# Kernel tuning notes

Measured on AMD Instinct MI355X. Metric: run time of the kernel, lower is better.

The kernel has to match this reference:

```python
import jax, jax.numpy as jnp
import numpy as np

N_NODES = 100000
N_EDGES = 1600000
IN_SIZE = 512
HID_SIZE = 256
OUT_SIZE = 16
DROP_P = 0.5


def _degrees(idx, n):
    d = jax.ops.segment_sum(jnp.ones(idx.shape[0], jnp.float32), idx, num_segments=n)
    return jnp.maximum(d, 1.0)  # DGL clamps zero degrees to 1


def graph_conv(src, dst, feat, W, b, activation=None):
    # DGL GraphConv, norm='both': D_in^{-1/2} A D_out^{-1/2} X W + b
    n = feat.shape[0]
    inv_sqrt_dout = _degrees(src, n) ** -0.5   # out-degree of source nodes
    inv_sqrt_din = _degrees(dst, n) ** -0.5    # in-degree of destination nodes
    h = feat * inv_sqrt_dout[:, None]
    h = h @ W  # in_feats >= out_feats -> transform before aggregation (same math)
    # message passing: scatter-add source messages to destinations
    h = jax.ops.segment_sum(h[src], dst, num_segments=n)
    h = h * inv_sqrt_din[:, None] + b
    if activation is not None:
        h = activation(h)
    return h


def setup_inputs() -> dict:
    key = jax.random.key(0)
    ks = jax.random.split(key, 9)
    features = jax.random.normal(ks[0], (N_NODES, IN_SIZE), jnp.float32)
    src = jax.random.randint(ks[1], (N_EDGES,), 0, N_NODES)
    dst = jax.random.randint(ks[2], (N_EDGES,), 0, N_NODES)
    W1 = jax.random.normal(ks[3], (IN_SIZE, HID_SIZE), jnp.float32) / np.sqrt(IN_SIZE).astype(np.float32)
    b1 = jnp.zeros((HID_SIZE,), jnp.float32)
    W2 = jax.random.normal(ks[4], (HID_SIZE, HID_SIZE), jnp.float32) / np.sqrt(HID_SIZE).astype(np.float32)
    b2 = jnp.zeros((HID_SIZE,), jnp.float32)
    W3 = jax.random.normal(ks[5], (HID_SIZE, OUT_SIZE), jnp.float32) / np.sqrt(HID_SIZE).astype(np.float32)
    b3 = jnp.zeros((OUT_SIZE,), jnp.float32)
    return {"features": features, "src": src, "dst": dst,
            "W1": W1, "b1": b1, "W2": W2, "b2": b2, "W3": W3, "b3": b3}


def reference(features, src, dst, W1, b1, W2, b2, W3, b3):
    # layer 0: GraphConv + relu
    h = graph_conv(src, dst, features, W1, b1, activation=jax.nn.relu)
    # dropout(0.5) before layer 1 (deterministic fixed-key mask, training semantics)
    keep = jax.random.bernoulli(jax.random.key(42), 1.0 - DROP_P, h.shape)
    h = jnp.where(keep, h / (1.0 - DROP_P), 0.0)
    # layer 1: GraphConv (no activation)
    h = graph_conv(src, dst, h, W2, b2, activation=None)
    # layer 2: plain Linear head
    return h @ W3 + b3
```

## Files before the change

kernel.cpp:

```cpp
#include <hip/hip_runtime.h>
#include <stdint.h>

#define NN    100000
#define NE    1600000
#define IN_F  512
#define HID   256
#define OUTF  16
#define NPAD  100096
#define NBK   391
#define EPB   8192

typedef unsigned int u32;
typedef __bf16 bfrag  __attribute__((ext_vector_type(8)));
typedef float  f32x4  __attribute__((ext_vector_type(4)));
typedef short  s16x8  __attribute__((ext_vector_type(8)));

__device__ __forceinline__ u32 rotl32(u32 x, int r){ return (x<<r)|(x>>(32-r)); }

__device__ __forceinline__ bool drop_keep(u32 i){
    const u32 ks0 = 0u, ks1 = 42u, ks2 = 0x1BD11BDAu ^ 0u ^ 42u;
    u32 x0 = 0u + ks0;
    u32 x1 = i  + ks1;
#define TFR(r) { x0 += x1; x1 = rotl32(x1,(r)); x1 ^= x0; }
    TFR(13) TFR(15) TFR(26) TFR(6)   x0 += ks1; x1 += ks2 + 1u;
    TFR(17) TFR(29) TFR(16) TFR(24)  x0 += ks2; x1 += ks0 + 2u;
    TFR(13) TFR(15) TFR(26) TFR(6)   x0 += ks0; x1 += ks1 + 3u;
    TFR(17) TFR(29) TFR(16) TFR(24)  x0 += ks1; x1 += ks2 + 4u;
    TFR(13) TFR(15) TFR(26) TFR(6)   x0 += ks2; x1 += ks0 + 5u;
#undef TFR
    return ((x0 ^ x1) >> 31) == 0u;
}

__device__ __forceinline__ short f2b(float f){
    union { float f; u32 u; } v; v.f = f;
    u32 r = (v.u + 0x7FFFu + ((v.u >> 16) & 1u)) >> 16;
    return (short)r;
}
__device__ __forceinline__ float blo(u32 u){ union{u32 u; float f;} v; v.u = u << 16;         return v.f; }
__device__ __forceinline__ float bhi(u32 u){ union{u32 u; float f;} v; v.u = u & 0xFFFF0000u; return v.f; }

__device__ __forceinline__ u32 cvt_pk_bf16(float lo, float hi){
    u32 r;
    asm("v_cvt_pk_bf16_f32 %0, %1, %2" : "=v"(r) : "v"(lo), "v"(hi));
    return r;
}

__device__ __forceinline__ void gll16(const void* g, void* l){
    __builtin_amdgcn_global_load_lds((const __attribute__((address_space(1))) void*)g,
                                     (__attribute__((address_space(3))) void*)l, 16, 0, 0);
}


__global__ __launch_bounds__(256) void build_hist(const int4* __restrict__ src4,
                                                  const int4* __restrict__ dst4,
                                                  int* deg_out, int* __restrict__ bcnt){
    __shared__ int h[NBK];
    int t = threadIdx.x;
    for (int i = t; i < NBK; i += 256) h[i] = 0;
    __syncthreads();
    for (int i = blockIdx.x * 256 + t; i < NE / 4; i += gridDim.x * 256) {
        int4 s = src4[i];
        int4 d = dst4[i];
        atomicAdd(&deg_out[s.x], 1);
        atomicAdd(&deg_out[s.y], 1);
        atomicAdd(&deg_out[s.z], 1);
        atomicAdd(&deg_out[s.w], 1);
        atomicAdd(&h[d.x >> 8], 1);
        atomicAdd(&h[d.y >> 8], 1);
        atomicAdd(&h[d.z >> 8], 1);
        atomicAdd(&h[d.w >> 8], 1);
    }
    __syncthreads();
    for (int i = t; i < NBK; i += 256)
        if (h[i]) atomicAdd(&bcnt[i], h[i]);
}

__global__ __launch_bounds__(256) void finalize_deg(const int* __restrict__ deg_out,
                                                    const int* __restrict__ row_ptr,
                                                    float* isdo, float* isdi){
    int i = blockIdx.x * blockDim.x + threadIdx.x;
    if (i < NN) {
        isdo[i] = rsqrtf(fmaxf((float)deg_out[i], 1.0f));
        isdi[i] = rsqrtf(fmaxf((float)(row_ptr[i + 1] - row_ptr[i]), 1.0f));
    }
}

__global__ __launch_bounds__(512) void bucket_scan(const int* __restrict__ bcnt,
                                                   int* __restrict__ bbase,
                                                   int* __restrict__ bcur,
                                                   int* __restrict__ row_ptr){
    __shared__ int sh[512];
    int t = threadIdx.x;
    int v = (t < NBK) ? bcnt[t] : 0;
    sh[t] = v;
    __syncthreads();
    for (int off = 1; off < 512; off <<= 1) {
        int a = (t >= off) ? sh[t - off] : 0;
        __syncthreads();
        sh[t] += a;
        __syncthreads();
    }
    int excl = sh[t] - v;
    if (t < NBK) { bbase[t] = excl; bcur[t] = excl; }
    if (t == 0)  { bbase[NBK] = NE; row_ptr[NN] = NE; }
}

__global__ __launch_bounds__(256) void bucket_scatter(const int* __restrict__ src,
                                                      const int* __restrict__ dst,
                                                      int* bcur, u32* __restrict__ tmp){
    __shared__ int lh[NBK];
    __shared__ int lb[NBK];
    int t = threadIdx.x;
    for (int i = t; i < NBK; i += 256) lh[i] = 0;
    __syncthreads();
    const int e0 = blockIdx.x * EPB;
    for (int k = t * 4; k < EPB; k += 1024) {
        int e = e0 + k;
        if (e < NE) {
            int4 d = *(const int4*)(dst + e);
            atomicAdd(&lh[d.x >> 8], 1);
            atomicAdd(&lh[d.y >> 8], 1);
            atomicAdd(&lh[d.z >> 8], 1);
            atomicAdd(&lh[d.w >> 8], 1);
        }
    }
    __syncthreads();
    for (int i = t; i < NBK; i += 256) {
        int c = lh[i];
        if (c) lb[i] = atomicAdd(&bcur[i], c);
        lh[i] = 0;
    }
    __syncthreads();
    for (int k = t * 4; k < EPB; k += 1024) {
        int e = e0 + k;
        if (e < NE) {
            int4 d = *(const int4*)(dst + e);
            int4 s = *(const int4*)(src + e);
            int b0 = d.x >> 8, b1 = d.y >> 8, b2 = d.z >> 8, b3 = d.w >> 8;
            int r0 = atomicAdd(&lh[b0], 1);
            tmp[lb[b0] + r0] = ((u32)s.x << 8) | ((u32)d.x & 255u);
            int r1 = atomicAdd(&lh[b1], 1);
            tmp[lb[b1] + r1] = ((u32)s.y << 8) | ((u32)d.y & 255u);
            int r2 = atomicAdd(&lh[b2], 1);
            tmp[lb[b2] + r2] = ((u32)s.z << 8) | ((u32)d.z & 255u);
            int r3 = atomicAdd(&lh[b3], 1);
            tmp[lb[b3] + r3] = ((u32)s.w << 8) | ((u32)d.w & 255u);
        }
    }
}

__global__ __launch_bounds__(256) void bucket_finalize(const u32* __restrict__ tmp,
                                                       const int* __restrict__ bbase,
                                                       int* __restrict__ row_ptr,
                                                       int* __restrict__ col_src){
    __shared__ int h[256];
    __shared__ int wtot[4];
    const int t = threadIdx.x;
    const int b = blockIdx.x;
    const int base = bbase[b];
    const int cnt  = bbase[b + 1] - base;
    h[t] = 0;
    __syncthreads();
    for (int k = t; k < cnt; k += 256)
        atomicAdd(&h[tmp[base + k] & 255u], 1);
    __syncthreads();
    int v = h[t];
    int lane = t & 63, w = t >> 6;
    int s = v;
    #pragma unroll
    for (int off = 1; off < 64; off <<= 1) {
        int u = __shfl_up(s, off);
        if (lane >= off) s += u;
    }
    if (lane == 63) wtot[w] = s;
    __syncthreads();
    int woff = 0;
    #pragma unroll
    for (int i = 0; i < 4; ++i) woff += (i < w) ? wtot[i] : 0;
    int excl = woff + s - v;
    int d = (b << 8) + t;
    if (d < NN) row_ptr[d] = base + excl;
    h[t] = excl;
    __syncthreads();
    for (int k = t; k < cnt; k += 256) {
        u32 p = tmp[base + k];
        int r = atomicAdd(&h[p & 255u], 1);
        col_src[base + r] = (int)(p >> 8);
    }
}


template<int Kd, int Nd>
__global__ __launch_bounds__(256) void convert_wt(const float* __restrict__ W,
                                                  short* __restrict__ WT){
    int i = blockIdx.x * 256 + threadIdx.x;
    if (i >= Kd * Nd) return;
    int n = i / Kd, k = i - n * Kd;
    WT[i] = f2b(W[(size_t)k * Nd + n]);
}

__global__ __launch_bounds__(256) void gemm_x(const float* __restrict__ X,
                                              const short* __restrict__ BT,
                                              const float* __restrict__ isdo,
                                              short* __restrict__ C){
    __shared__ __align__(16) float As[2 * 4160];
    __shared__ __align__(16) short Bs[2 * 8320];

    const int t = threadIdx.x;
    const int wave = t >> 6, lane = t & 63;
    const int bm = blockIdx.x * 128;

    const float* paA[4];
    #pragma unroll
    for (int g = 0; g < 4; ++g) {
        int row = bm + wave * 32 + g * 8 + (lane >> 3);
        if (row > NN - 1) row = NN - 1;
        paA[g] = X + (size_t)row * IN_F + (lane & 7) * 4;
    }
    const short* paB[4];
    #pragma unroll
    for (int g = 0; g < 4; ++g) {
        int col = (wave * 4 + g) * 16 + (lane >> 2);
        paB[g] = BT + (size_t)col * IN_F + (lane & 3) * 8;
    }

    const int wr = (wave >> 1) * 64;
    const int wc = (wave & 1) * 128;
    const int kq = lane >> 4, r15 = lane & 15;

    f32x4 acc[4][8];
    #pragma unroll
    for (int m = 0; m < 4; ++m)
        #pragma unroll
        for (int n = 0; n < 8; ++n) acc[m][n] = (f32x4)0.0f;

#define STAGE_X(BUF, K0) { \
    float* dA = As + (BUF) * 4160 + wave * 1040; \
    gll16(paA[0] + (K0), dA);       gll16(paA[1] + (K0), dA + 260); \
    gll16(paA[2] + (K0), dA + 520); gll16(paA[3] + (K0), dA + 780); \
    short* dB = Bs + (BUF) * 8320 + wave * 2080; \
    gll16(paB[0] + (K0), dB);        gll16(paB[1] + (K0), dB + 520); \
    gll16(paB[2] + (K0), dB + 1040); gll16(paB[3] + (K0), dB + 1560); }

#define COMPUTE_X(BUF) { \
    const float* AsC = As + (BUF) * 4160; \
    const short* BsC = Bs + (BUF) * 8320; \
    bfrag af[4], bfg[8]; \
    _Pragma("unroll") \
    for (int m = 0; m < 4; ++m) { \
        int r  = wr + m * 16 + r15; \
        const float* ap = AsC + (r >> 3) * 260 + (r & 7) * 32 + kq * 8; \
        float4 f0 = *(const float4*)ap; \
        float4 f1 = *(const float4*)(ap + 4); \
        uint4 q = make_uint4(cvt_pk_bf16(f0.x, f0.y), cvt_pk_bf16(f0.z, f0.w), \
                             cvt_pk_bf16(f1.x, f1.y), cvt_pk_bf16(f1.z, f1.w)); \
        af[m] = *(bfrag*)&q; \
    } \
    _Pragma("unroll") \
    for (int n = 0; n < 8; ++n) { \
        int cg = (wc >> 4) + n; \
        bfg[n] = *(const bfrag*)(BsC + cg * 520 + r15 * 32 + kq * 8); \
    } \
    _Pragma("unroll") \
    for (int m = 0; m < 4; ++m) \
        _Pragma("unroll") \
        for (int n = 0; n < 8; ++n) \
            acc[m][n] = __builtin_amdgcn_mfma_f32_16x16x32_bf16(af[m], bfg[n], acc[m][n], 0, 0, 0); }

    const int NT = IN_F / 32;
    STAGE_X(0, 0);
    int cur = 0;
    for (int tt = 0; tt < NT - 1; ++tt) {
        STAGE_X(cur ^ 1, (tt + 1) * 32);
        asm volatile("s_waitcnt vmcnt(8)" ::: "memory");
        __builtin_amdgcn_s_barrier();
        COMPUTE_X(cur);
        asm volatile("" ::: "memory");
        __builtin_amdgcn_s_barrier();
        cur ^= 1;
    }
    asm volatile("s_waitcnt vmcnt(0)" ::: "memory");
    __builtin_amdgcn_s_barrier();
    COMPUTE_X(cur);
#undef STAGE_X
#undef COMPUTE_X

    const int crow0 = bm + wr + (lane >> 4) * 4;
    const int ccol0 = wc + r15;
    #pragma unroll
    for (int m = 0; m < 4; ++m)
        #pragma unroll
        for (int r = 0; r < 4; ++r) {
            int row = crow0 + m * 16 + r;
            float sc = (row < NN) ? isdo[row] : 0.0f;
            #pragma unroll
            for (int n = 0; n < 8; ++n)
                C[(size_t)row * HID + ccol0 + n * 16] = f2b(acc[m][n][r] * sc);
        }
}

template<int K>
__global__ __launch_bounds__(256) void gemm_bt(const short* __restrict__ A,
                                               const short* __restrict__ BT,
                                               short* __restrict__ C){
    __shared__ __align__(16) short As[2 * 4160];
    __shared__ __align__(16) short Bs[2 * 8320];

    const int t = threadIdx.x;
    const int wave = t >> 6, lane = t & 63;
    const int bm = blockIdx.x * 128;

    const short* paA[2];
    #pragma unroll
    for (int g = 0; g < 2; ++g) {
        int row = bm + (wave * 2 + g) * 16 + (lane >> 2);
        paA[g] = A + (size_t)row * K + (lane & 3) * 8;
    }
    const short* paB[4];
    #pragma unroll
    for (int g = 0; g < 4; ++g) {
        int col = (wave * 4 + g) * 16 + (lane >> 2);
        paB[g] = BT + (size_t)col * K + (lane & 3) * 8;
    }

    const int wr = (wave >> 1) * 64;
    const int wc = (wave & 1) * 128;
    const int kq = lane >> 4, r15 = lane & 15;

    f32x4 acc[4][8];
    #pragma unroll
    for (int m = 0; m < 4; ++m)
        #pragma unroll
        for (int n = 0; n < 8; ++n) acc[m][n] = (f32x4)0.0f;

#define STAGE_B(BUF, K0) { \
    short* dA = As + (BUF) * 4160 + wave * 1040; \
    gll16(paA[0] + (K0), dA); gll16(paA[1] + (K0), dA + 520); \
    short* dB = Bs + (BUF) * 8320 + wave * 2080; \
    gll16(paB[0] + (K0), dB);        gll16(paB[1] + (K0), dB + 520); \
    gll16(paB[2] + (K0), dB + 1040); gll16(paB[3] + (K0), dB + 1560); }

#define COMPUTE_B(BUF) { \
    const short* AsC = As + (BUF) * 4160; \
    const short* BsC = Bs + (BUF) * 8320; \
    bfrag af[4], bfg[8]; \
    _Pragma("unroll") \
    for (int m = 0; m < 4; ++m) { \
        int ch = (wr + m * 16) >> 4; \
        af[m] = *(const bfrag*)(AsC + ch * 520 + r15 * 32 + kq * 8); \
    } \
    _Pragma("unroll") \
    for (int n = 0; n < 8; ++n) { \
        int cg = (wc >> 4) + n; \
        bfg[n] = *(const bfrag*)(BsC + cg * 520 + r15 * 32 + kq * 8); \
    } \
    _Pragma("unroll") \
    for (int m = 0; m < 4; ++m) \
        _Pragma("unroll") \
        for (int n = 0; n < 8; ++n) \
            acc[m][n] = __builtin_amdgcn_mfma_f32_16x16x32_bf16(af[m], bfg[n], acc[m][n], 0, 0, 0); }

    const int NT = K / 32;
    STAGE_B(0, 0);
    int cur = 0;
    for (int tt = 0; tt < NT - 1; ++tt) {
        STAGE_B(cur ^ 1, (tt + 1) * 32);
        asm volatile("s_waitcnt vmcnt(6)" ::: "memory");
        __builtin_amdgcn_s_barrier();
        COMPUTE_B(cur);
        asm volatile("" ::: "memory");
        __builtin_amdgcn_s_barrier();
        cur ^= 1;
    }
    asm volatile("s_waitcnt vmcnt(0)" ::: "memory");
    __builtin_amdgcn_s_barrier();
    COMPUTE_B(cur);
#undef STAGE_B
#undef COMPUTE_B

    const int crow0 = bm + wr + (lane >> 4) * 4;
    const int ccol0 = wc + r15;
    #pragma unroll
    for (int m = 0; m < 4; ++m)
        #pragma unroll
        for (int n = 0; n < 8; ++n)
            #pragma unroll
            for (int r = 0; r < 4; ++r)
                C[(size_t)(crow0 + m * 16 + r) * HID + ccol0 + n * 16] = f2b(acc[m][n][r]);
}

template<int MODE>
__global__ __launch_bounds__(256) void gather_agg(const short* __restrict__ H,
                                                  const int* __restrict__ rp,
                                                  const int* __restrict__ cs,
                                                  const float* __restrict__ isdi,
                                                  const float* __restrict__ isdo,
                                                  const float* __restrict__ bias,
                                                  short* __restrict__ out){
    const int lane = threadIdx.x & 63;
    const int node = __builtin_amdgcn_readfirstlane((int)(blockIdx.x * 4) + (int)(threadIdx.x >> 6));
    const int e0  = rp[node];
    const int end = rp[node + 1];
    const int sub = lane & 31, half = lane >> 5;
    const u32 off16 = (u32)sub * 16u;
    const char* Hb = (const char*)H;

    float a[8] = {0,0,0,0,0,0,0,0};
    float b[8] = {0,0,0,0,0,0,0,0};

#define LD4(s) (*(const uint4*)(Hb + ((((u32)(s)) << 9) | off16)))
#define ACC(A, u) { A[0]+=blo(u.x); A[1]+=bhi(u.x); A[2]+=blo(u.y); A[3]+=bhi(u.y); \
                    A[4]+=blo(u.z); A[5]+=bhi(u.z); A[6]+=blo(u.w); A[7]+=bhi(u.w); }

    int eb = e0;
    for (; eb + 16 <= end; eb += 16) {
        int t0 = cs[eb+0],  t1 = cs[eb+1],  t2 = cs[eb+2],  t3 = cs[eb+3];
        int t4 = cs[eb+4],  t5 = cs[eb+5],  t6 = cs[eb+6],  t7 = cs[eb+7];
        int t8 = cs[eb+8],  t9 = cs[eb+9],  tA = cs[eb+10], tB = cs[eb+11];
        int tC = cs[eb+12], tD = cs[eb+13], tE = cs[eb+14], tF = cs[eb+15];
        int s0 = half ? t1 : t0;
        int s1 = half ? t3 : t2;
        int s2 = half ? t5 : t4;
        int s3 = half ? t7 : t6;
        int s4 = half ? t9 : t8;
        int s5 = half ? tB : tA;
        int s6 = half ? tD : tC;
        int s7 = half ? tF : tE;
        uint4 u0 = LD4(s0), u1 = LD4(s1), u2 = LD4(s2), u3 = LD4(s3);
        uint4 u4 = LD4(s4), u5 = LD4(s5), u6 = LD4(s6), u7 = LD4(s7);
        ACC(a, u0); ACC(b, u1); ACC(a, u2); ACC(b, u3);
        ACC(a, u4); ACC(b, u5); ACC(a, u6); ACC(b, u7);
    }
    for (; eb + 8 <= end; eb += 8) {
        int t0 = cs[eb+0], t1 = cs[eb+1], t2 = cs[eb+2], t3 = cs[eb+3];
        int t4 = cs[eb+4], t5 = cs[eb+5], t6 = cs[eb+6], t7 = cs[eb+7];
        int s0 = half ? t1 : t0;
        int s1 = half ? t3 : t2;
        int s2 = half ? t5 : t4;
        int s3 = half ? t7 : t6;
        uint4 u0 = LD4(s0), u1 = LD4(s1), u2 = LD4(s2), u3 = LD4(s3);
        ACC(a, u0); ACC(b, u1); ACC(a, u2); ACC(b, u3);
    }
    for (; eb + 2 <= end; eb += 2) {
        int t0 = cs[eb], t1 = cs[eb+1];
        int s = half ? t1 : t0;
        uint4 u = LD4(s);
        ACC(a, u);
    }
    if (eb < end) {
        int s = cs[eb];
        uint4 u = LD4(s);
        if (half == 0) { ACC(a, u); }
    }
#undef ACC
#undef LD4
    #pragma unroll
    for (int j = 0; j < 8; ++j) a[j] += b[j];

    const int srcl = lane >> 1;
    const bool oddq = (lane & 1) != 0;
    float v[4];
    #pragma unroll
    for (int j = 0; j < 4; ++j) {
        float p0 = __shfl(a[j],     srcl);
        float p1 = __shfl(a[j + 4], srcl);
        float q0 = __shfl(a[j],     srcl + 32);
        float q1 = __shfl(a[j + 4], srcl + 32);
        v[j] = oddq ? (p1 + q1) : (p0 + q0);
    }

    float sd = isdi[node];
    float4 bb = *(const float4*)(bias + lane * 4);
    float h0 = v[0] * sd + bb.x;
    float h1 = v[1] * sd + bb.y;
    float h2 = v[2] * sd + bb.z;
    float h3 = v[3] * sd + bb.w;

    if (MODE == 0) {
        float so2 = 2.0f * isdo[node];
        u32 base = (u32)node * HID + (u32)lane * 4;
        h0 = drop_keep(base + 0) ? fmaxf(h0, 0.f) * so2 : 0.f;
        h1 = drop_keep(base + 1) ? fmaxf(h1, 0.f) * so2 : 0.f;
        h2 = drop_keep(base + 2) ? fmaxf(h2, 0.f) * so2 : 0.f;
        h3 = drop_keep(base + 3) ? fmaxf(h3, 0.f) * so2 : 0.f;
    }

    uint2 wv;
    wv.x = ((u32)(unsigned short)f2b(h1) << 16) | (u32)(unsigned short)f2b(h0);
    wv.y = ((u32)(unsigned short)f2b(h3) << 16) | (u32)(unsigned short)f2b(h2);
    *(uint2*)((char*)out + (size_t)node * 512 + (u32)lane * 8u) = wv;
}

__global__ __launch_bounds__(256) void head_kernel(const short* __restrict__ H2,
                                                   const float* __restrict__ W3,
                                                   const float* __restrict__ b3,
                                                   float* __restrict__ out){
    __shared__ float W3s[HID * OUTF];
    __shared__ short rows[16][HID + 8];
    int t = threadIdx.x;
    for (int i = t; i < HID * OUTF; i += 256) W3s[i] = W3[i];
    const int n0 = blockIdx.x * 16;
    for (int c = t; c < 16 * 32; c += 256) {
        int r = c >> 5, cc = c & 31;
        *(s16x8*)(&rows[r][cc * 8]) = *(const s16x8*)(H2 + (size_t)(n0 + r) * HID + cc * 8);
    }
    __syncthreads();
    int nl = t >> 4, k = t & 15;
    float acc = 0.0f;
    #pragma unroll 4
    for (int j = 0; j < HID; ++j)
        acc += blo((u32)(unsigned short)rows[nl][j]) * W3s[j * OUTF + k];
    out[(size_t)(n0 + nl) * OUTF + k] = acc + b3[k];
}

extern "C" void kernel_launch(void* const* d_in, const int* in_sizes, int n_in,
                              void* d_out, int out_size, void* d_ws, size_t ws_size,
                              hipStream_t stream) {
    const float* X   = (const float*)d_in[0];
    const int*   src = (const int*)  d_in[1];
    const int*   dst = (const int*)  d_in[2];
    const float* W1  = (const float*)d_in[3];
    const float* b1  = (const float*)d_in[4];
    const float* W2  = (const float*)d_in[5];
    const float* b2  = (const float*)d_in[6];
    const float* W3  = (const float*)d_in[7];
    const float* b3  = (const float*)d_in[8];
    float* out = (float*)d_out;

    char* ws = (char*)d_ws;
    size_t o = 0;
    int*   deg_out = (int*)  (ws + o); o += (size_t)NN * 4;
    int*   bcnt    = (int*)  (ws + o); o += (size_t)NBK * 4;
    float* isdo    = (float*)(ws + o); o += (size_t)NN * 4;
    float* isdi    = (float*)(ws + o); o += (size_t)NN * 4;
    int*   row_ptr = (int*)  (ws + o); o += (size_t)(NN + 1) * 4;
    int*   bbase   = (int*)  (ws + o); o += (size_t)(NBK + 1) * 4;
    int*   bcur    = (int*)  (ws + o); o += (size_t)NBK * 4;
    int*   col_src = (int*)  (ws + o); o += (size_t)NE * 4;
    o = (o + 255) & ~(size_t)255;
    short* W1t = (short*)(ws + o); o += (size_t)IN_F * HID * 2;
    short* W2t = (short*)(ws + o); o += (size_t)HID * HID * 2;
    o = (o + 255) & ~(size_t)255;
    short* hA    = (short*)(ws + o); o += (size_t)NPAD * HID * 2;
    short* hB    = (short*)(ws + o); o += (size_t)NPAD * HID * 2;
    short* h2pre = (short*)(ws + o); o += (size_t)NPAD * HID * 2;
    if (ws_size < o) return;
    short* h2  = hA;
    u32*   tmp = (u32*)hB;

    const size_t zlen = (size_t)NN * 4 + (size_t)NBK * 4;
    hipMemsetAsync(deg_out, 0, zlen, stream);

    build_hist<<<256, 256, 0, stream>>>((const int4*)src, (const int4*)dst, deg_out, bcnt);
    bucket_scan<<<1, 512, 0, stream>>>(bcnt, bbase, bcur, row_ptr);
    bucket_scatter<<<(NE + EPB - 1) / EPB, 256, 0, stream>>>(src, dst, bcur, tmp);
    bucket_finalize<<<NBK, 256, 0, stream>>>(tmp, bbase, row_ptr, col_src);
    finalize_deg<<<(NN + 255) / 256, 256, 0, stream>>>(deg_out, row_ptr, isdo, isdi);

    convert_wt<IN_F, HID><<<IN_F * HID / 256, 256, 0, stream>>>(W1, W1t);
    convert_wt<HID, HID><<<HID * HID / 256, 256, 0, stream>>>(W2, W2t);

    gemm_x<<<NPAD / 128, 256, 0, stream>>>(X, W1t, isdo, hA);
    gather_agg<0><<<NN / 4, 256, 0, stream>>>(hA, row_ptr, col_src, isdi, isdo, b1, hB);

    gemm_bt<HID><<<NPAD / 128, 256, 0, stream>>>(hB, W2t, h2pre);
    gather_agg<1><<<NN / 4, 256, 0, stream>>>(h2pre, row_ptr, col_src, isdi, isdo, b2, h2);

    head_kernel<<<NN / 16, 256, 0, stream>>>(h2, W3, b3, out);
}
```

Measured before the change: 487.0 us.

## Split gather aggregation into column slices with 8-edge-parallel waves

Restructures the neighbor aggregation so each block handles one 64-column slice of 32 nodes, with each wave processing 8 edges concurrently (one 8-lane group per edge) over 8 nodes sequentially. Lane-group partial sums are combined with xor shuffles, and dropout masks are computed once per lane and shared via a ballot instead of four hash evaluations per lane. This aims to raise memory-level parallelism on the irregular row gathers and cut RNG work, at the cost of narrower 128-byte row accesses and rereading edge indices once per slice.

New measurement: 529.9 us. 8.8% more time.

```diff
diff --git a/kernel.cpp b/kernel.cpp
--- a/kernel.cpp
+++ b/kernel.cpp
@@ -398,97 +398,91 @@
                                                   const float* __restrict__ bias,
                                                   short* __restrict__ out){
     const int lane = threadIdx.x & 63;
-    const int node = __builtin_amdgcn_readfirstlane((int)(blockIdx.x * 4) + (int)(threadIdx.x >> 6));
-    const int e0  = rp[node];
-    const int end = rp[node + 1];
-    const int sub = lane & 31, half = lane >> 5;
-    const u32 off16 = (u32)sub * 16u;
+    const int wv   = __builtin_amdgcn_readfirstlane((int)(threadIdx.x >> 6));
+    const int s    = (int)(blockIdx.x & 3);
+    const int bg   = (int)(blockIdx.x >> 2);
+    const int eg   = lane >> 3;
+    const int p    = lane & 7;
+    const u32 off  = (u32)(s * 128 + p * 16);
     const char* Hb = (const char*)H;
 
-    float a[8] = {0,0,0,0,0,0,0,0};
-    float b[8] = {0,0,0,0,0,0,0,0};
-
-#define LD4(s) (*(const uint4*)(Hb + ((((u32)(s)) << 9) | off16)))
+    const float4 bb0 = *(const float4*)(bias + s * 64 + p * 8);
+    const float4 bb1 = *(const float4*)(bias + s * 64 + p * 8 + 4);
+
+#define LD4(sv) (*(const uint4*)(Hb + ((((u32)(sv)) << 9) | off)))
 #define ACC(A, u) { A[0]+=blo(u.x); A[1]+=bhi(u.x); A[2]+=blo(u.y); A[3]+=bhi(u.y); \
                     A[4]+=blo(u.z); A[5]+=bhi(u.z); A[6]+=blo(u.w); A[7]+=bhi(u.w); }
 
-    int eb = e0;
-    for (; eb + 16 <= end; eb += 16) {
-        int t0 = cs[eb+0],  t1 = cs[eb+1],  t2 = cs[eb+2],  t3 = cs[eb+3];
-        int t4 = cs[eb+4],  t5 = cs[eb+5],  t6 = cs[eb+6],  t7 = cs[eb+7];
-        int t8 = cs[eb+8],  t9 = cs[eb+9],  tA = cs[eb+10], tB = cs[eb+11];
-        int tC = cs[eb+12], tD = cs[eb+13], tE = cs[eb+14], tF = cs[eb+15];
-        int s0 = half ? t1 : t0;
-        int s1 = half ? t3 : t2;
-        int s2 = half ? t5 : t4;
-        int s3 = half ? t7 : t6;
-        int s4 = half ? t9 : t8;
-        int s5 = half ? tB : tA;
-        int s6 = half ? tD : tC;
-        int s7 = half ? tF : tE;
-        uint4 u0 = LD4(s0), u1 = LD4(s1), u2 = LD4(s2), u3 = LD4(s3);
-        uint4 u4 = LD4(s4), u5 = LD4(s5), u6 = LD4(s6), u7 = LD4(s7);
-        ACC(a, u0); ACC(b, u1); ACC(a, u2); ACC(b, u3);
-        ACC(a, u4); ACC(b, u5); ACC(a, u6); ACC(b, u7);
-    }
-    for (; eb + 8 <= end; eb += 8) {
-        int t0 = cs[eb+0], t1 = cs[eb+1], t2 = cs[eb+2], t3 = cs[eb+3];
-        int t4 = cs[eb+4], t5 = cs[eb+5], t6 = cs[eb+6], t7 = cs[eb+7];
-        int s0 = half ? t1 : t0;
-        int s1 = half ? t3 : t2;
-        int s2 = half ? t5 : t4;
-        int s3 = half ? t7 : t6;
-        uint4 u0 = LD4(s0), u1 = LD4(s1), u2 = LD4(s2), u3 = LD4(s3);
-        ACC(a, u0); ACC(b, u1); ACC(a, u2); ACC(b, u3);
-    }
-    for (; eb + 2 <= end; eb += 2) {
-        int t0 = cs[eb], t1 = cs[eb+1];
-        int s = half ? t1 : t0;
-        uint4 u = LD4(s);
-        ACC(a, u);
-    }
-    if (eb < end) {
-        int s = cs[eb];
-        uint4 u = LD4(s);
-        if (half == 0) { ACC(a, u); }
+    for (int nn = 0; nn < 8; ++nn) {
+        const int node = bg * 32 + wv * 8 + nn;
+        const int e0  = rp[node];
+        const int end = rp[node + 1];
+
+        float a[8] = {0,0,0,0,0,0,0,0};
+        float b[8] = {0,0,0,0,0,0,0,0};
+
+        int eb = e0;
+        for (; eb + 16 <= end; eb += 16) {
+            int i0 = cs[eb + eg];
+            int i1 = cs[eb + 8 + eg];
+            uint4 u0 = LD4(i0);
+            uint4 u1 = LD4(i1);
+            ACC(a, u0);
+            ACC(b, u1);
+        }
+        if (eb < end) {
+            const int last = end - 1;
+            int ex = eb + eg;
+            int i0 = cs[ex < end ? ex : last];
+            uint4 u0 = LD4(i0);
+            if (ex >= end) u0 = make_uint4(0u, 0u, 0u, 0u);
+            ACC(a, u0);
+            if (eb + 8 < end) {
+                int ey = eb + 8 + eg;
+                int i1 = cs[ey < end ? ey : last];
+                uint4 u1 = LD4(i1);
+                if (ey >= end) u1 = make_uint4(0u, 0u, 0u, 0u);
+                ACC(b, u1);
+            }
+        }
+        #pragma unroll
+        for (int j = 0; j < 8; ++j) a[j] += b[j];
+
+        #pragma unroll
+        for (int j = 0; j < 8; ++j) {
+            a[j] += __shfl_xor(a[j], 8);
+            a[j] += __shfl_xor(a[j], 16);
+            a[j] += __shfl_xor(a[j], 32);
+        }
+
+        float sd = isdi[node];
+        float h[8];
+        h[0] = a[0] * sd + bb0.x;  h[1] = a[1] * sd + bb0.y;
+        h[2] = a[2] * sd + bb0.z;  h[3] = a[3] * sd + bb0.w;
+        h[4] = a[4] * sd + bb1.x;  h[5] = a[5] * sd + bb1.y;
+        h[6] = a[6] * sd + bb1.z;  h[7] = a[7] * sd + bb1.w;
+
+        if (MODE == 0) {
+            unsigned long long mask =
+                __ballot(drop_keep((u32)node * HID + (u32)s * 64 + (u32)lane));
+            float so2 = 2.0f * isdo[node];
+            #pragma unroll
+            for (int j = 0; j < 8; ++j) {
+                bool keep = (mask >> (p * 8 + j)) & 1ull;
+                h[j] = keep ? fmaxf(h[j], 0.0f) * so2 : 0.0f;
+            }
+        }
+
+        uint4 wvv;
+        wvv.x = ((u32)(unsigned short)f2b(h[1]) << 16) | (u32)(unsigned short)f2b(h[0]);
+        wvv.y = ((u32)(unsigned short)f2b(h[3]) << 16) | (u32)(unsigned short)f2b(h[2]);
+        wvv.z = ((u32)(unsigned short)f2b(h[5]) << 16) | (u32)(unsigned short)f2b(h[4]);
+        wvv.w = ((u32)(unsigned short)f2b(h[7]) << 16) | (u32)(unsigned short)f2b(h[6]);
+        if (lane < 8)
+            *(uint4*)((char*)out + (size_t)node * 512 + (u32)(s * 128 + lane * 16)) = wvv;
     }
 #undef ACC
 #undef LD4
-    #pragma unroll
-    for (int j = 0; j < 8; ++j) a[j] += b[j];
-
-    const int srcl = lane >> 1;
-    const bool oddq = (lane & 1) != 0;
-    float v[4];
-    #pragma unroll
-    for (int j = 0; j < 4; ++j) {
-        float p0 = __shfl(a[j],     srcl);
-        float p1 = __shfl(a[j + 4], srcl);
-        float q0 = __shfl(a[j],     srcl + 32);
-        float q1 = __shfl(a[j + 4], srcl + 32);
-        v[j] = oddq ? (p1 + q1) : (p0 + q0);
-    }
-
-    float sd = isdi[node];
-    float4 bb = *(const float4*)(bias + lane * 4);
-    float h0 = v[0] * sd + bb.x;
-    float h1 = v[1] * sd + bb.y;
-    float h2 = v[2] * sd + bb.z;
-    float h3 = v[3] * sd + bb.w;
-
-    if (MODE == 0) {
-        float so2 = 2.0f * isdo[node];
-        u32 base = (u32)node * HID + (u32)lane * 4;
-        h0 = drop_keep(base + 0) ? fmaxf(h0, 0.f) * so2 : 0.f;
-        h1 = drop_keep(base + 1) ? fmaxf(h1, 0.f) * so2 : 0.f;
-        h2 = drop_keep(base + 2) ? fmaxf(h2, 0.f) * so2 : 0.f;
-        h3 = drop_keep(base + 3) ? fmaxf(h3, 0.f) * so2 : 0.f;
-    }
-
-    uint2 wv;
-    wv.x = ((u32)(unsigned short)f2b(h1) << 16) | (u32)(unsigned short)f2b(h0);
-    wv.y = ((u32)(unsigned short)f2b(h3) << 16) | (u32)(unsigned short)f2b(h2);
-    *(uint2*)((char*)out + (size_t)node * 512 + (u32)lane * 8u) = wv;
 }
 
 __global__ __launch_bounds__(256) void head_kernel(const short* __restrict__ H2,
@@ -560,11 +554,13 @@
     convert_wt<IN_F, HID><<<IN_F * HID / 256, 256, 0, stream>>>(W1, W1t);
     convert_wt<HID, HID><<<HID * HID / 256, 256, 0, stream>>>(W2, W2t);
 
+    const int GGRID = 4 * (NN / 32);
+
     gemm_x<<<NPAD / 128, 256, 0, stream>>>(X, W1t, isdo, hA);
-    gather_agg<0><<<NN / 4, 256, 0, stream>>>(hA, row_ptr, col_src, isdi, isdo, b1, hB);
+    gather_agg<0><<<GGRID, 256, 0, stream>>>(hA, row_ptr, col_src, isdi, isdo, b1, hB);
 
     gemm_bt<HID><<<NPAD / 128, 256, 0, stream>>>(hB, W2t, h2pre);
-    gather_agg<1><<<NN / 4, 256, 0, stream>>>(h2pre, row_ptr, col_src, isdi, isdo, b2, h2);
+    gather_agg<1><<<GGRID, 256, 0, stream>>>(h2pre, row_ptr, col_src, isdi, isdo, b2, h2);
 
     head_kernel<<<NN / 16, 256, 0, stream>>>(h2, W3, b3, out);
 }
```

## Fuse second-layer aggregation with linear head and tile weight transpose

Applied to the files above, without the earlier changes.

The second gather-aggregate now feeds its per-node hidden row straight into the 256x16 output projection in shared memory. This removes the intermediate h2 buffer write and read, plus a separate head kernel launch. The cost is that every block stages a transposed W3 into shared memory and adds a short reduction tail. Weight conversion also switches to a shared-memory tiled transpose so that both global reads and writes are coalesced.

Result: faster. 456.1 us (-6.3%).

```diff
diff --git a/kernel.cpp b/kernel.cpp
--- a/kernel.cpp
+++ b/kernel.cpp
@@ -191,12 +191,18 @@
 
 
 template<int Kd, int Nd>
-__global__ __launch_bounds__(256) void convert_wt(const float* __restrict__ W,
-                                                  short* __restrict__ WT){
-    int i = blockIdx.x * 256 + threadIdx.x;
-    if (i >= Kd * Nd) return;
-    int n = i / Kd, k = i - n * Kd;
-    WT[i] = f2b(W[(size_t)k * Nd + n]);
+__global__ __launch_bounds__(256) void convert_wt_t(const float* __restrict__ W,
+                                                    short* __restrict__ WT){
+    __shared__ float tile[64][65];
+    const int t = threadIdx.x;
+    const int k0 = (int)(blockIdx.x % (Kd / 64)) * 64;
+    const int n0 = (int)(blockIdx.x / (Kd / 64)) * 64;
+    const int c = t & 63;
+    for (int r = t >> 6; r < 64; r += 4)
+        tile[r][c] = W[(size_t)(k0 + r) * Nd + n0 + c];
+    __syncthreads();
+    for (int rn = t >> 6; rn < 64; rn += 4)
+        WT[(size_t)(n0 + rn) * Kd + k0 + c] = f2b(tile[c][rn]);
 }
 
 __global__ __launch_bounds__(256) void gemm_x(const float* __restrict__ X,
@@ -389,14 +395,13 @@
                 C[(size_t)(crow0 + m * 16 + r) * HID + ccol0 + n * 16] = f2b(acc[m][n][r]);
 }
 
-template<int MODE>
-__global__ __launch_bounds__(256) void gather_agg(const short* __restrict__ H,
-                                                  const int* __restrict__ rp,
-                                                  const int* __restrict__ cs,
-                                                  const float* __restrict__ isdi,
-                                                  const float* __restrict__ isdo,
-                                                  const float* __restrict__ bias,
-                                                  short* __restrict__ out){
+__global__ __launch_bounds__(256) void gather_agg0(const short* __restrict__ H,
+                                                   const int* __restrict__ rp,
+                                                   const int* __restrict__ cs,
+                                                   const float* __restrict__ isdi,
+                                                   const float* __restrict__ isdo,
+                                                   const float* __restrict__ bias,
+                                                   short* __restrict__ out){
     const int lane = threadIdx.x & 63;
     const int node = __builtin_amdgcn_readfirstlane((int)(blockIdx.x * 4) + (int)(threadIdx.x >> 6));
     const int e0  = rp[node];
@@ -476,14 +481,12 @@
     float h2 = v[2] * sd + bb.z;
     float h3 = v[3] * sd + bb.w;
 
-    if (MODE == 0) {
-        float so2 = 2.0f * isdo[node];
-        u32 base = (u32)node * HID + (u32)lane * 4;
-        h0 = drop_keep(base + 0) ? fmaxf(h0, 0.f) * so2 : 0.f;
-        h1 = drop_keep(base + 1) ? fmaxf(h1, 0.f) * so2 : 0.f;
-        h2 = drop_keep(base + 2) ? fmaxf(h2, 0.f) * so2 : 0.f;
-        h3 = drop_keep(base + 3) ? fmaxf(h3, 0.f) * so2 : 0.f;
-    }
+    float so2 = 2.0f * isdo[node];
+    u32 base = (u32)node * HID + (u32)lane * 4;
+    h0 = drop_keep(base + 0) ? fmaxf(h0, 0.f) * so2 : 0.f;
+    h1 = drop_keep(base + 1) ? fmaxf(h1, 0.f) * so2 : 0.f;
+    h2 = drop_keep(base + 2) ? fmaxf(h2, 0.f) * so2 : 0.f;
+    h3 = drop_keep(base + 3) ? fmaxf(h3, 0.f) * so2 : 0.f;
 
     uint2 wv;
     wv.x = ((u32)(unsigned short)f2b(h1) << 16) | (u32)(unsigned short)f2b(h0);
@@ -491,26 +494,125 @@
     *(uint2*)((char*)out + (size_t)node * 512 + (u32)lane * 8u) = wv;
 }
 
-__global__ __launch_bounds__(256) void head_kernel(const short* __restrict__ H2,
+__global__ __launch_bounds__(256) void gather_head(const short* __restrict__ H,
+                                                   const int* __restrict__ rp,
+                                                   const int* __restrict__ cs,
+                                                   const float* __restrict__ isdi,
+                                                   const float* __restrict__ bias,
                                                    const float* __restrict__ W3,
                                                    const float* __restrict__ b3,
                                                    float* __restrict__ out){
-    __shared__ float W3s[HID * OUTF];
-    __shared__ short rows[16][HID + 8];
-    int t = threadIdx.x;
-    for (int i = t; i < HID * OUTF; i += 256) W3s[i] = W3[i];
-    const int n0 = blockIdx.x * 16;
-    for (int c = t; c < 16 * 32; c += 256) {
-        int r = c >> 5, cc = c & 31;
-        *(s16x8*)(&rows[r][cc * 8]) = *(const s16x8*)(H2 + (size_t)(n0 + r) * HID + cc * 8);
-    }
-    __syncthreads();
-    int nl = t >> 4, k = t & 15;
-    float acc = 0.0f;
-    #pragma unroll 4
-    for (int j = 0; j < HID; ++j)
-        acc += blo((u32)(unsigned short)rows[nl][j]) * W3s[j * OUTF + k];
-    out[(size_t)(n0 + nl) * OUTF + k] = acc + b3[k];
+    __shared__ float W3t[OUTF][HID + 4];
+    __shared__ float hs[4][HID];
+
+    const int t = threadIdx.x;
+    {
+        const float4* wrow = (const float4*)(W3 + (size_t)t * OUTF);
+        float4 w0 = wrow[0], w1 = wrow[1], w2 = wrow[2], w3 = wrow[3];
+        W3t[ 0][t] = w0.x; W3t[ 1][t] = w0.y; W3t[ 2][t] = w0.z; W3t[ 3][t] = w0.w;
+        W3t[ 4][t] = w1.x; W3t[ 5][t] = w1.y; W3t[ 6][t] = w1.z; W3t[ 7][t] = w1.w;
+        W3t[ 8][t] = w2.x; W3t[ 9][t] = w2.y; W3t[10][t] = w2.z; W3t[11][t] = w2.w;
+        W3t[12][t] = w3.x; W3t[13][t] = w3.y; W3t[14][t] = w3.z; W3t[15][t] = w3.w;
+    }
+    __syncthreads();
+
+    const int lane = threadIdx.x & 63;
+    const int wave = (int)(threadIdx.x >> 6);
+    const int node = __builtin_amdgcn_readfirstlane((int)(blockIdx.x * 4) + wave);
+    const int e0  = rp[node];
+    const int end = rp[node + 1];
+    const int sub = lane & 31, half = lane >> 5;
+    const u32 off16 = (u32)sub * 16u;
+    const char* Hb = (const char*)H;
+
+    float a[8] = {0,0,0,0,0,0,0,0};
+    float b[8] = {0,0,0,0,0,0,0,0};
+
+#define LD4(s) (*(const uint4*)(Hb + ((((u32)(s)) << 9) | off16)))
+#define ACC(A, u) { A[0]+=blo(u.x); A[1]+=bhi(u.x); A[2]+=blo(u.y); A[3]+=bhi(u.y); \
+                    A[4]+=blo(u.z); A[5]+=bhi(u.z); A[6]+=blo(u.w); A[7]+=bhi(u.w); }
+
+    int eb = e0;
+    for (; eb + 16 <= end; eb += 16) {
+        int t0 = cs[eb+0],  t1 = cs[eb+1],  t2 = cs[eb+2],  t3 = cs[eb+3];
+        int t4 = cs[eb+4],  t5 = cs[eb+5],  t6 = cs[eb+6],  t7 = cs[eb+7];
+        int t8 = cs[eb+8],  t9 = cs[eb+9],  tA = cs[eb+10], tB = cs[eb+11];
+        int tC = cs[eb+12], tD = cs[eb+13], tE = cs[eb+14], tF = cs[eb+15];
+        int s0 = half ? t1 : t0;
+        int s1 = half ? t3 : t2;
+        int s2 = half ? t5 : t4;
+        int s3 = half ? t7 : t6;
+        int s4 = half ? t9 : t8;
+        int s5 = half ? tB : tA;
+        int s6 = half ? tD : tC;
+        int s7 = half ? tF : tE;
+        uint4 u0 = LD4(s0), u1 = LD4(s1), u2 = LD4(s2), u3 = LD4(s3);
+        uint4 u4 = LD4(s4), u5 = LD4(s5), u6 = LD4(s6), u7 = LD4(s7);
+        ACC(a, u0); ACC(b, u1); ACC(a, u2); ACC(b, u3);
+        ACC(a, u4); ACC(b, u5); ACC(a, u6); ACC(b, u7);
+    }
+    for (; eb + 8 <= end; eb += 8) {
+        int t0 = cs[eb+0], t1 = cs[eb+1], t2 = cs[eb+2], t3 = cs[eb+3];
+        int t4 = cs[eb+4], t5 = cs[eb+5], t6 = cs[eb+6], t7 = cs[eb+7];
+        int s0 = half ? t1 : t0;
+        int s1 = half ? t3 : t2;
+        int s2 = half ? t5 : t4;
+        int s3 = half ? t7 : t6;
+        uint4 u0 = LD4(s0), u1 = LD4(s1), u2 = LD4(s2), u3 = LD4(s3);
+        ACC(a, u0); ACC(b, u1); ACC(a, u2); ACC(b, u3);
+    }
+    for (; eb + 2 <= end; eb += 2) {
+        int t0 = cs[eb], t1 = cs[eb+1];
+        int s = half ? t1 : t0;
+        uint4 u = LD4(s);
+        ACC(a, u);
+    }
+    if (eb < end) {
+        int s = cs[eb];
+        uint4 u = LD4(s);
+        if (half == 0) { ACC(a, u); }
+    }
+#undef ACC
+#undef LD4
+    #pragma unroll
+    for (int j = 0; j < 8; ++j) a[j] += b[j];
+
+    const int srcl = lane >> 1;
+    const bool oddq = (lane & 1) != 0;
+    float v[4];
+    #pragma unroll
+    for (int j = 0; j < 4; ++j) {
+        float p0 = __shfl(a[j],     srcl);
+        float p1 = __shfl(a[j + 4], srcl);
+        float q0 = __shfl(a[j],     srcl + 32);
+        float q1 = __shfl(a[j + 4], srcl + 32);
+        v[j] = oddq ? (p1 + q1) : (p0 + q0);
+    }
+
+    float sd = isdi[node];
+    float4 bb = *(const float4*)(bias + lane * 4);
+    float4 hq;
+    hq.x = v[0] * sd + bb.x;
+    hq.y = v[1] * sd + bb.y;
+    hq.z = v[2] * sd + bb.z;
+    hq.w = v[3] * sd + bb.w;
+
+    *(float4*)&hs[wave][lane * 4] = hq;
+    const int k   = lane & 15;
+    const int grp = lane >> 4;
+    const float* hrow = &hs[wave][grp * 64];
+    const float* wrow = &W3t[k][grp * 64];
+    float p = 0.0f;
+    #pragma unroll
+    for (int c4 = 0; c4 < 16; ++c4) {
+        float4 hv = *(const float4*)(hrow + c4 * 4);
+        float4 wv = *(const float4*)(wrow + c4 * 4);
+        p += hv.x * wv.x + hv.y * wv.y + hv.z * wv.z + hv.w * wv.w;
+    }
+    p += __shfl_xor(p, 16);
+    p += __shfl_xor(p, 32);
+    if (lane < 16)
+        out[(size_t)node * OUTF + lane] = p + b3[lane];
 }
 
 extern "C" void kernel_launch(void* const* d_in, const int* in_sizes, int n_in,
@@ -545,8 +647,7 @@
     short* hB    = (short*)(ws + o); o += (size_t)NPAD * HID * 2;
     short* h2pre = (short*)(ws + o); o += (size_t)NPAD * HID * 2;
     if (ws_size < o) return;
-    short* h2  = hA;
-    u32*   tmp = (u32*)hB;
+    u32* tmp = (u32*)hB;
 
     const size_t zlen = (size_t)NN * 4 + (size_t)NBK * 4;
     hipMemsetAsync(deg_out, 0, zlen, stream);
@@ -557,14 +658,13 @@
     bucket_finalize<<<NBK, 256, 0, stream>>>(tmp, bbase, row_ptr, col_src);
     finalize_deg<<<(NN + 255) / 256, 256, 0, stream>>>(deg_out, row_ptr, isdo, isdi);
 
-    convert_wt<IN_F, HID><<<IN_F * HID / 256, 256, 0, stream>>>(W1, W1t);
-    convert_wt<HID, HID><<<HID * HID / 256, 256, 0, stream>>>(W2, W2t);
+    convert_wt_t<IN_F, HID><<<(IN_F / 64) * (HID / 64), 256, 0, stream>>>(W1, W1t);
+    convert_wt_t<HID, HID><<<(HID / 64) * (HID / 64), 256, 0, stream>>>(W2, W2t);
 
     gemm_x<<<NPAD / 128, 256, 0, stream>>>(X, W1t, isdo, hA);
-    gather_agg<0><<<NN / 4, 256, 0, stream>>>(hA, row_ptr, col_src, isdi, isdo, b1, hB);
+    gather_agg0<<<NN / 4, 256, 0, stream>>>(hA, row_ptr, col_src, isdi, isdo, b1, hB);
 
     gemm_bt<HID><<<NPAD / 128, 256, 0, stream>>>(hB, W2t, h2pre);
-    gather_agg<1><<<NN / 4, 256, 0, stream>>>(h2pre, row_ptr, col_src, isdi, isdo, b2, h2);
-
-    head_kernel<<<NN / 16, 256, 0, stream>>>(h2, W3, b3, out);
-}
+
+    gather_head<<<NN / 4, 256, 0, stream>>>(h2pre, row_ptr, col_src, isdi, b2, W3, b3, out);
+}
```
